# Kernel tuning notes

Hardware: AMD Instinct MI355X
Metric: run time of the kernel (lower is better)

## Reference

```python
import jax, jax.numpy as jnp
import numpy as np


def setup_inputs() -> dict:
    key = jax.random.key(0)
    k1, = jax.random.split(key, 1)
    B, L, D = 128, 1024, 768
    hidden_states = jax.random.normal(k1, (B, L, D), dtype=jnp.float32)
    attention_mask = jnp.zeros((B, 1, 1, L), dtype=jnp.float32)
    return {"hidden_states": hidden_states, "attention_mask": attention_mask, "K": 512}


def reference(hidden_states, attention_mask, K):
    B, L, D = hidden_states.shape
    # r tokens to merge, protected class token (ToMe: r = min(r, (t - protected)//2))
    r = max(0, L - K)
    r = min(r, (L - 1) // 2)

    # --- bipartite soft matching (indices computed under no_grad in torch) ---
    metric = hidden_states / jnp.linalg.norm(hidden_states, axis=-1, keepdims=True)
    a = metric[:, ::2, :]   # [B, t1, D] even tokens (src side)
    b = metric[:, 1::2, :]  # [B, t2, D] odd tokens (dst side)
    scores = jnp.einsum('bid,bjd->bij', a, b)  # [B, t1, t2]
    scores = scores.at[:, 0, :].set(-jnp.inf)  # protect class token (row 0 of src)
    node_max = jnp.max(scores, axis=-1)        # [B, t1]
    node_idx = jnp.argmax(scores, axis=-1)     # [B, t1] best dst per src
    order = jnp.argsort(-node_max, axis=-1)    # descending similarity
    src_idx = order[:, :r]                     # [B, r] tokens to merge away
    unm_idx = jnp.sort(order[:, r:], axis=-1)  # [B, t1-r] kept src tokens (sorted: class_token=True)
    dst_idx = jnp.take_along_axis(node_idx, src_idx, axis=-1)  # [B, r]

    # --- merge(x, mode='mean') with include_self=True ---
    src = hidden_states[:, ::2, :]   # [B, t1, D]
    dst = hidden_states[:, 1::2, :]  # [B, t2, D]
    t2 = dst.shape[1]
    unm = jnp.take_along_axis(src, unm_idx[..., None], axis=1)     # [B, t1-r, D]
    src_g = jnp.take_along_axis(src, src_idx[..., None], axis=1)   # [B, r, D]
    bidx = jnp.arange(B)[:, None]
    dst_sum = dst.at[bidx, dst_idx].add(src_g)                     # self + merged srcs
    counts = jnp.ones((B, t2), dtype=hidden_states.dtype).at[bidx, dst_idx].add(1.0)
    dst_mean = dst_sum / counts[..., None]

    preserved_tokens = jnp.concatenate([unm, dst_mean], axis=1)    # [B, t1-r+t2, D]
    final_attention_mask = jnp.zeros((B, 1, 1, preserved_tokens.shape[1]),
                                     dtype=hidden_states.dtype)
    return preserved_tokens, final_attention_mask
```

## Files before the change

### kernel.cpp

```cpp
#include <hip/hip_runtime.h>
#include <hip/hip_bf16.h>

#define B_ 128
#define L_ 1024
#define T_ 512
#define D_ 768
#define CH_ 96
#define DT_ 513
#define TAU_C 1e-3f
#define PBUF_ 1024

#define KS_B_CSTR 8208
#define KS_B_BYTES (4 * KS_B_CSTR)
#define KS_A_CSTR 1040
#define KS_A_BYTES (4 * KS_A_CSTR)
#define KS_BYTES (KS_B_BYTES + KS_A_BYTES)
#define SMEM_BYTES (4 * KS_BYTES)

typedef __attribute__((ext_vector_type(8))) short bf16x8;
typedef __attribute__((ext_vector_type(4))) float f32x4;

typedef const __attribute__((address_space(1))) unsigned int* gas1_t;
typedef __attribute__((address_space(3))) unsigned int* gas3_t;

__device__ __forceinline__ unsigned short f2bf_rne(float x){
    unsigned u = __float_as_uint(x);
    unsigned r = (u + 0x7FFFu + ((u >> 16) & 1u)) >> 16;
    return (unsigned short)r;
}

__global__ __launch_bounds__(256) void pack_k(const float* __restrict__ hs,
                                              unsigned short* __restrict__ Apk,
                                              unsigned short* __restrict__ Bpk,
                                              double* __restrict__ nsq,
                                              int* __restrict__ paircnt){
    __shared__ __align__(16) unsigned short LhS[CH_ * 16 * 8];
    if (blockIdx.x == 0 && threadIdx.x == 0) *paircnt = 0;
    int b = blockIdx.x >> 6, g = blockIdx.x & 63;
    int wv = threadIdx.x >> 6, lane = threadIdx.x & 63;

    #pragma unroll
    for (int rr = 0; rr < 4; ++rr){
        int jj = wv * 4 + rr;
        long seq = (long)b * L_ + g * 16 + jj;
        const float4* src = (const float4*)(hs + seq * D_);
        float4 f0 = src[lane], f1 = src[lane + 64], f2 = src[lane + 128];
        double s = 0.0;
        s += (double)f0.x*f0.x + (double)f0.y*f0.y + (double)f0.z*f0.z + (double)f0.w*f0.w;
        s += (double)f1.x*f1.x + (double)f1.y*f1.y + (double)f1.z*f1.z + (double)f1.w*f1.w;
        s += (double)f2.x*f2.x + (double)f2.y*f2.y + (double)f2.z*f2.z + (double)f2.w*f2.w;
        #pragma unroll
        for (int off = 32; off; off >>= 1) s += __shfl_xor(s, off);
        if (lane == 0 && (jj & 1)) nsq[seq] = s;
        float rn = (float)(1.0 / sqrt(s));
        float4 fv[3] = {f0, f1, f2};
        #pragma unroll
        for (int t = 0; t < 3; ++t){
            int e0 = t * 256 + lane * 4;
            int c = e0 >> 3, ei = e0 & 7;
            float vv[4] = {fv[t].x, fv[t].y, fv[t].z, fv[t].w};
            short4 hv;
            #pragma unroll
            for (int e = 0; e < 4; ++e)
                ((short*)&hv)[e] = (short)f2bf_rne(vv[e] * rn);
            int o = c * 128 + ((jj ^ (c & 7)) << 3) + ei;
            *(short4*)(LhS + o) = hv;
        }
    }
    __syncthreads();
    #pragma unroll
    for (int it = 0; it < 6; ++it){
        int linear = it * 256 + threadIdx.x;
        int c = linear >> 4, jj = linear & 15;
        int o = c * 128 + ((jj ^ (c & 7)) << 3);
        int tok = g * 8 + (jj >> 1);
        long go = ((long)(b * CH_ + c) * T_ + tok) * 8;
        if (jj & 1) *(bf16x8*)(Bpk + go) = *(const bf16x8*)(LhS + o);
        else        *(bf16x8*)(Apk + go) = *(const bf16x8*)(LhS + o);
    }
}

__global__ __launch_bounds__(512, 2) void coarse_k(const unsigned short* __restrict__ Apk,
                                                   const unsigned short* __restrict__ Bpk,
                                                   int* __restrict__ node_idx,
                                                   unsigned long long* __restrict__ rowkey,
                                                   int* __restrict__ paircnt,
                                                   int2* __restrict__ pairs){
    __shared__ __align__(16) char SMEM[SMEM_BYTES];

    int bid = blockIdx.x;
    int xcd = bid & 7, q = bid >> 3;
    int it = q & 7, bhi = q >> 3;
    int b = xcd + 8 * bhi;

    int tid = threadIdx.x;
    int w = tid >> 6, lane = tid & 63, l15 = lane & 15, l4 = lane >> 4;

    long pkbase = (long)b * CH_ * T_;
    int ca = w >> 1, tb4a = (w & 1) << 1;

    #define STAGE(s_, slot_) do {                                                          \
        char* dst_ = SMEM + (slot_) * KS_BYTES;                                            \
        _Pragma("unroll")                                                                  \
        for (int n_ = 0; n_ < 4; ++n_){                                                    \
            const unsigned short* sp_ = Bpk + (pkbase + (long)((s_)*4 + n_) * T_ + w * 64 + lane) * 8; \
            __builtin_amdgcn_global_load_lds((gas1_t)sp_, (gas3_t)(dst_ + n_ * KS_B_CSTR + w * 1024), 16, 0, 0); \
        }                                                                                  \
        _Pragma("unroll")                                                                  \
        for (int n_ = 0; n_ < 2; ++n_){                                                    \
            int tb_ = tb4a + n_;                                                           \
            const unsigned short* sp_ = Apk + (pkbase + (long)((s_)*4 + ca) * T_ + it * 64 + tb_ * 16) * 8 + lane * 2; \
            __builtin_amdgcn_global_load_lds((gas1_t)sp_, (gas3_t)(dst_ + KS_B_BYTES + ca * KS_A_CSTR + tb_ * 256), 4, 0, 0); \
        }                                                                                  \
    } while (0)

    STAGE(0, 0); STAGE(1, 1); STAGE(2, 2);

    f32x4 acc[4][4];
    #pragma unroll
    for (int i = 0; i < 4; ++i)
        #pragma unroll
        for (int j = 0; j < 4; ++j) acc[i][j] = (f32x4){0.f, 0.f, 0.f, 0.f};

    __syncthreads();

    #pragma unroll 4
    for (int s = 0; s < 24; ++s){
        if (s < 21) STAGE(s + 3, (s + 3) & 3);
        const char* slot = SMEM + (s & 3) * KS_BYTES;
        bf16x8 ah[4], bh[4];
        #pragma unroll
        for (int ib = 0; ib < 4; ++ib)
            ah[ib] = *(const bf16x8*)(slot + KS_B_BYTES + l4 * KS_A_CSTR + (ib * 16 + l15) * 16);
        #pragma unroll
        for (int jb = 0; jb < 4; ++jb)
            bh[jb] = *(const bf16x8*)(slot + l4 * KS_B_CSTR + (w * 64 + jb * 16 + l15) * 16);
        __builtin_amdgcn_s_setprio(1);
        #pragma unroll
        for (int jb = 0; jb < 4; ++jb)
            #pragma unroll
            for (int ib = 0; ib < 4; ++ib)
                acc[ib][jb] = __builtin_amdgcn_mfma_f32_16x16x32_bf16(ah[ib], bh[jb], acc[ib][jb], 0, 0, 0);
        __builtin_amdgcn_s_setprio(0);
        if (s <= 20)      asm volatile("s_waitcnt vmcnt(12)" ::: "memory");
        else if (s == 21) asm volatile("s_waitcnt vmcnt(6)"  ::: "memory");
        else              asm volatile("s_waitcnt vmcnt(0)"  ::: "memory");
        __builtin_amdgcn_s_barrier();
        asm volatile("" ::: "memory");
    }
    #undef STAGE

    float* pm1s = (float*)SMEM;
    int*   pjs  = (int*)(SMEM + 2048);
    float* m1f  = (float*)(SMEM + 4096);
    int*   cnd  = (int*)(SMEM + 4352);
    int2*  pbuf = (int2*)(SMEM + 4608);
    int*   pcnt_s  = (int*)(SMEM + 12800);
    int*   pbase_s = (int*)(SMEM + 12804);

    #pragma unroll
    for (int ib = 0; ib < 4; ++ib)
        #pragma unroll
        for (int rr = 0; rr < 4; ++rr){
            float m1 = -1e30f; int j1 = 0;
            #pragma unroll
            for (int jb = 0; jb < 4; ++jb){
                float v = acc[ib][jb][rr];
                int col = w * 64 + jb * 16 + l15;
                if (v > m1){ m1 = v; j1 = col; }
            }
            #pragma unroll
            for (int m = 1; m < 16; m <<= 1){
                float o1 = __shfl_xor(m1, m);
                int   oj = __shfl_xor(j1, m);
                if (o1 > m1 || (o1 == m1 && oj < j1)){ m1 = o1; j1 = oj; }
            }
            if (l15 == 0){
                int row = ib * 16 + l4 * 4 + rr;
                pm1s[row * 8 + w] = m1; pjs[row * 8 + w] = j1;
            }
        }
    __syncthreads();
    int grow0 = b * T_ + it * 64;
    if (tid < 64){
        float M1 = -1e30f; int J1 = 0;
        #pragma unroll
        for (int w2 = 0; w2 < 8; ++w2){
            float a1 = pm1s[tid * 8 + w2]; int aj = pjs[tid * 8 + w2];
            if (a1 > M1 || (a1 == M1 && aj < J1)){ M1 = a1; J1 = aj; }
        }
        node_idx[grow0 + tid] = J1;
        m1f[tid] = M1;
        cnd[tid] = 0;
        rowkey[grow0 + tid] = 0ULL;
        if (tid == 0) *pcnt_s = 0;
    }
    __syncthreads();
    #pragma unroll
    for (int ib = 0; ib < 4; ++ib)
        #pragma unroll
        for (int rr = 0; rr < 4; ++rr){
            int row = ib * 16 + l4 * 4 + rr;
            float thr_ = m1f[row] - TAU_C;
            int hits = 0;
            #pragma unroll
            for (int jb = 0; jb < 4; ++jb) hits += (acc[ib][jb][rr] > thr_) ? 1 : 0;
            #pragma unroll
            for (int m = 1; m < 16; m <<= 1) hits += __shfl_xor(hits, m);
            if (l15 == 0 && hits) atomicAdd(&cnd[row], hits);
        }
    __syncthreads();
    #pragma unroll
    for (int ib = 0; ib < 4; ++ib)
        #pragma unroll
        for (int rr = 0; rr < 4; ++rr){
            int row = ib * 16 + l4 * 4 + rr;
            if (cnd[row] < 2) continue;
            if (it == 0 && row == 0) continue;
            float thr_ = m1f[row] - TAU_C;
            #pragma unroll
            for (int jb = 0; jb < 4; ++jb)
                if (acc[ib][jb][rr] > thr_){
                    int idx = atomicAdd(pcnt_s, 1);
                    int2 pr = make_int2(grow0 + row, w * 64 + jb * 16 + l15);
                    if (idx < PBUF_) pbuf[idx] = pr;
                    else { int p = atomicAdd(paircnt, 1); pairs[p] = pr; }
                }
        }
    __syncthreads();
    if (tid == 0) *pbase_s = atomicAdd(paircnt, min(*pcnt_s, PBUF_));
    __syncthreads();
    int n = min(*pcnt_s, PBUF_);
    for (int k2 = tid; k2 < n; k2 += 512) pairs[*pbase_s + k2] = pbuf[k2];
}

__global__ __launch_bounds__(256) void refine_k(const float* __restrict__ hs,
                                                const double* __restrict__ nsq,
                                                const int* __restrict__ paircnt,
                                                const int2* __restrict__ pairs,
                                                unsigned long long* __restrict__ rowkey){
    int n = *paircnt;
    int w = threadIdx.x >> 6, lane = threadIdx.x & 63;
    for (int p = blockIdx.x * 4 + w; p < n; p += gridDim.x * 4){
        int2 pr = pairs[p];
        int grow = pr.x, j = pr.y;
        int b = grow >> 9, i = grow & 511;
        const float* ar = hs + ((long)b * L_ + 2 * i) * D_;
        const float* br = hs + ((long)b * L_ + 2 * j + 1) * D_;
        double s = 0.0;
        #pragma unroll
        for (int dd = 0; dd < 12; ++dd){
            int d = dd * 64 + lane;
            s += (double)ar[d] * (double)br[d];
        }
        #pragma unroll
        for (int off = 32; off; off >>= 1) s += __shfl_xor(s, off);
        if (lane == 0){
            double sc = s / sqrt(nsq[(long)b * L_ + 2 * j + 1]);
            unsigned long long bits = (unsigned long long)__double_as_longlong(sc);
            unsigned long long key = (bits >> 63) ? ~bits : (bits | 0x8000000000000000ULL);
            key = (key & ~0xFFFFULL) | (unsigned long long)(511 - j);
            atomicMax(&rowkey[grow], key);
        }
    }
}

__global__ __launch_bounds__(512) void csr_k(const int* __restrict__ node_idx,
                                             const unsigned long long* __restrict__ rowkey,
                                             int* __restrict__ goff,
                                             int* __restrict__ glist){
    __shared__ int sidx[512];
    __shared__ int off[513];
    __shared__ int tmp[512];
    __shared__ int cnt[512];
    int b = blockIdx.x, t = threadIdx.x;
    unsigned long long rk = rowkey[b * T_ + t];
    sidx[t] = rk ? (511 - (int)(rk & 0xFFFFULL)) : node_idx[b * T_ + t];
    cnt[t] = 0;
    __syncthreads();
    if (t >= 1) atomicAdd(&cnt[sidx[t]], 1);
    __syncthreads();
    tmp[t] = cnt[t];
    __syncthreads();
    for (int s = 1; s < 512; s <<= 1){
        int v = (t >= s) ? tmp[t - s] : 0;
        __syncthreads();
        tmp[t] += v;
        __syncthreads();
    }
    if (t == 0) off[0] = 0;
    off[t + 1] = tmp[t];
    __syncthreads();
    if (t >= 1){
        int j = sidx[t], r = 0;
        for (int i2 = 1; i2 < t; ++i2) r += (sidx[i2] == j);
        glist[b * T_ + off[j] + r] = t;
    }
    goff[b * 513 + t] = off[t];
    if (t == 0) goff[b * 513 + 512] = off[512];
}

__global__ __launch_bounds__(192) void merge_k(const float* __restrict__ hs,
                                               const int* __restrict__ goff,
                                               const int* __restrict__ glist,
                                               float* __restrict__ out){
    int bid = blockIdx.x;
    int b = bid / DT_, jj = bid - b * DT_;
    long obase4 = ((long)b * DT_ + jj) * (D_ / 4);
    float4* out4 = (float4*)out;
    if (threadIdx.x == 0) out[(long)B_ * DT_ * D_ + b * DT_ + jj] = 0.0f;
    int d = threadIdx.x;
    if (jj == 0){
        const float4* src = (const float4*)(hs + (long)b * L_ * D_);
        out4[obase4 + d] = src[d];
        return;
    }
    int j = jj - 1;
    int o0 = goff[b * 513 + j], o1 = goff[b * 513 + j + 1];
    const float4* dst = (const float4*)(hs + ((long)b * L_ + 2 * j + 1) * D_);
    float4 a = dst[d];
    for (int s = o0; s < o1; ++s){
        int i = glist[b * T_ + s];
        const float4* srow = (const float4*)(hs + ((long)b * L_ + 2 * i) * D_);
        float4 v = srow[d];
        a.x += v.x; a.y += v.y; a.z += v.z; a.w += v.w;
    }
    float rc = 1.0f / (float)(o1 - o0 + 1);
    a.x *= rc; a.y *= rc; a.z *= rc; a.w *= rc;
    out4[obase4 + d] = a;
}

extern "C" void kernel_launch(void* const* d_in, const int* in_sizes, int n_in,
                              void* d_out, int out_size, void* d_ws, size_t ws_size,
                              hipStream_t stream){
    const float* hs = (const float*)d_in[0];
    float* out = (float*)d_out;
    char* ws = (char*)d_ws;

    const long PSZ = (long)B_ * CH_ * T_ * 8;
    unsigned short* Apk = (unsigned short*)ws;
    unsigned short* Bpk = Apk + PSZ;
    double* nsq      = (double*)(ws + 201326592);
    int*    node_idx = (int*)   (ws + 202375168);
    unsigned long long* rowkey = (unsigned long long*)(ws + 202637312);
    int*    paircnt  = (int*)   (ws + 203161600);
    int*    goff     = (int*)   (ws + 203161856);
    int*    glist    = (int*)   (ws + 203425024);
    int2*   pairs    = (int2*)  (ws + 203687168);

    pack_k  <<<B_ * 64, 256, 0, stream>>>(hs, Apk, Bpk, nsq, paircnt);
    coarse_k<<<B_ * 8, 512, 0, stream>>>(Apk, Bpk, node_idx, rowkey, paircnt, pairs);
    refine_k<<<512, 256, 0, stream>>>(hs, nsq, paircnt, pairs, rowkey);
    csr_k   <<<B_, 512, 0, stream>>>(node_idx, rowkey, goff, glist);
    merge_k <<<B_ * DT_, 192, 0, stream>>>(hs, goff, glist, out);
}
```

Measured before the change: 365.7 us.

## Enlarge coarse GEMM row tile to 128 with 2x4 wave grid and triple buffering

Each coarse_k block now handles 128 src rows instead of 64. The 8 waves form a 2x4 grid, each computing a 64x128 accumulator tile, so each B-chunk staged into LDS is reused across twice as many rows and the grid shrinks to 512 blocks. The A tile is loaded with 16-byte global_load_lds, and the pipeline drops from four stages to three to fit LDS, with the vmcnt waits adjusted to match. Doubling the accumulators raises register pressure and may hurt occupancy, and the shallower pipeline hides less load latency.

```diff
diff --git a/kernel.cpp b/kernel.cpp
--- a/kernel.cpp
+++ b/kernel.cpp
@@ -12,10 +12,10 @@
 
 #define KS_B_CSTR 8208
 #define KS_B_BYTES (4 * KS_B_CSTR)
-#define KS_A_CSTR 1040
+#define KS_A_CSTR 2064
 #define KS_A_BYTES (4 * KS_A_CSTR)
 #define KS_BYTES (KS_B_BYTES + KS_A_BYTES)
-#define SMEM_BYTES (4 * KS_BYTES)
+#define SMEM_BYTES (3 * KS_BYTES)
 
 typedef __attribute__((ext_vector_type(8))) short bf16x8;
 typedef __attribute__((ext_vector_type(4))) float f32x4;
@@ -90,14 +90,14 @@
 
     int bid = blockIdx.x;
     int xcd = bid & 7, q = bid >> 3;
-    int it = q & 7, bhi = q >> 3;
+    int it = q & 3, bhi = q >> 2;
     int b = xcd + 8 * bhi;
 
     int tid = threadIdx.x;
     int w = tid >> 6, lane = tid & 63, l15 = lane & 15, l4 = lane >> 4;
+    int wr = w >> 2, wc = w & 3;
 
     long pkbase = (long)b * CH_ * T_;
-    int ca = w >> 1, tb4a = (w & 1) << 1;
 
     #define STAGE(s_, slot_) do {                                                          \
         char* dst_ = SMEM + (slot_) * KS_BYTES;                                            \
@@ -106,45 +106,42 @@
             const unsigned short* sp_ = Bpk + (pkbase + (long)((s_)*4 + n_) * T_ + w * 64 + lane) * 8; \
             __builtin_amdgcn_global_load_lds((gas1_t)sp_, (gas3_t)(dst_ + n_ * KS_B_CSTR + w * 1024), 16, 0, 0); \
         }                                                                                  \
-        _Pragma("unroll")                                                                  \
-        for (int n_ = 0; n_ < 2; ++n_){                                                    \
-            int tb_ = tb4a + n_;                                                           \
-            const unsigned short* sp_ = Apk + (pkbase + (long)((s_)*4 + ca) * T_ + it * 64 + tb_ * 16) * 8 + lane * 2; \
-            __builtin_amdgcn_global_load_lds((gas1_t)sp_, (gas3_t)(dst_ + KS_B_BYTES + ca * KS_A_CSTR + tb_ * 256), 4, 0, 0); \
+        {                                                                                  \
+            const unsigned short* sp_ = Apk + (pkbase + (long)((s_)*4 + (w >> 1)) * T_ + it * 128 + (w & 1) * 64 + lane) * 8; \
+            __builtin_amdgcn_global_load_lds((gas1_t)sp_, (gas3_t)(dst_ + KS_B_BYTES + (w >> 1) * KS_A_CSTR + (w & 1) * 1024), 16, 0, 0); \
         }                                                                                  \
     } while (0)
 
-    STAGE(0, 0); STAGE(1, 1); STAGE(2, 2);
-
-    f32x4 acc[4][4];
+    STAGE(0, 0); STAGE(1, 1);
+
+    f32x4 acc[4][8];
     #pragma unroll
     for (int i = 0; i < 4; ++i)
         #pragma unroll
-        for (int j = 0; j < 4; ++j) acc[i][j] = (f32x4){0.f, 0.f, 0.f, 0.f};
-
-    __syncthreads();
-
-    #pragma unroll 4
+        for (int j = 0; j < 8; ++j) acc[i][j] = (f32x4){0.f, 0.f, 0.f, 0.f};
+
+    __syncthreads();
+
+    #pragma unroll 3
     for (int s = 0; s < 24; ++s){
-        if (s < 21) STAGE(s + 3, (s + 3) & 3);
-        const char* slot = SMEM + (s & 3) * KS_BYTES;
-        bf16x8 ah[4], bh[4];
+        if (s < 22) STAGE(s + 2, (s + 2) % 3);
+        const char* slot = SMEM + (s % 3) * KS_BYTES;
+        bf16x8 ah[4], bh[8];
         #pragma unroll
         for (int ib = 0; ib < 4; ++ib)
-            ah[ib] = *(const bf16x8*)(slot + KS_B_BYTES + l4 * KS_A_CSTR + (ib * 16 + l15) * 16);
-        #pragma unroll
-        for (int jb = 0; jb < 4; ++jb)
-            bh[jb] = *(const bf16x8*)(slot + l4 * KS_B_CSTR + (w * 64 + jb * 16 + l15) * 16);
+            ah[ib] = *(const bf16x8*)(slot + KS_B_BYTES + l4 * KS_A_CSTR + (wr * 64 + ib * 16 + l15) * 16);
+        #pragma unroll
+        for (int jb = 0; jb < 8; ++jb)
+            bh[jb] = *(const bf16x8*)(slot + l4 * KS_B_CSTR + (wc * 128 + jb * 16 + l15) * 16);
         __builtin_amdgcn_s_setprio(1);
         #pragma unroll
-        for (int jb = 0; jb < 4; ++jb)
+        for (int jb = 0; jb < 8; ++jb)
             #pragma unroll
             for (int ib = 0; ib < 4; ++ib)
                 acc[ib][jb] = __builtin_amdgcn_mfma_f32_16x16x32_bf16(ah[ib], bh[jb], acc[ib][jb], 0, 0, 0);
         __builtin_amdgcn_s_setprio(0);
-        if (s <= 20)      asm volatile("s_waitcnt vmcnt(12)" ::: "memory");
-        else if (s == 21) asm volatile("s_waitcnt vmcnt(6)"  ::: "memory");
-        else              asm volatile("s_waitcnt vmcnt(0)"  ::: "memory");
+        if (s < 22)      asm volatile("s_waitcnt vmcnt(5)" ::: "memory");
+        else             asm volatile("s_waitcnt vmcnt(0)" ::: "memory");
         __builtin_amdgcn_s_barrier();
         asm volatile("" ::: "memory");
     }
@@ -153,10 +150,10 @@
     float* pm1s = (float*)SMEM;
     int*   pjs  = (int*)(SMEM + 2048);
     float* m1f  = (float*)(SMEM + 4096);
-    int*   cnd  = (int*)(SMEM + 4352);
-    int2*  pbuf = (int2*)(SMEM + 4608);
-    int*   pcnt_s  = (int*)(SMEM + 12800);
-    int*   pbase_s = (int*)(SMEM + 12804);
+    int*   cnd  = (int*)(SMEM + 4608);
+    int2*  pbuf = (int2*)(SMEM + 5120);
+    int*   pcnt_s  = (int*)(SMEM + 13312);
+    int*   pbase_s = (int*)(SMEM + 13316);
 
     #pragma unroll
     for (int ib = 0; ib < 4; ++ib)
@@ -164,9 +161,9 @@
         for (int rr = 0; rr < 4; ++rr){
             float m1 = -1e30f; int j1 = 0;
             #pragma unroll
-            for (int jb = 0; jb < 4; ++jb){
+            for (int jb = 0; jb < 8; ++jb){
                 float v = acc[ib][jb][rr];
-                int col = w * 64 + jb * 16 + l15;
+                int col = wc * 128 + jb * 16 + l15;
                 if (v > m1){ m1 = v; j1 = col; }
             }
             #pragma unroll
@@ -176,17 +173,17 @@
                 if (o1 > m1 || (o1 == m1 && oj < j1)){ m1 = o1; j1 = oj; }
             }
             if (l15 == 0){
-                int row = ib * 16 + l4 * 4 + rr;
-                pm1s[row * 8 + w] = m1; pjs[row * 8 + w] = j1;
+                int row = wr * 64 + ib * 16 + l4 * 4 + rr;
+                pm1s[row * 4 + wc] = m1; pjs[row * 4 + wc] = j1;
             }
         }
     __syncthreads();
-    int grow0 = b * T_ + it * 64;
-    if (tid < 64){
+    int grow0 = b * T_ + it * 128;
+    if (tid < 128){
         float M1 = -1e30f; int J1 = 0;
         #pragma unroll
-        for (int w2 = 0; w2 < 8; ++w2){
-            float a1 = pm1s[tid * 8 + w2]; int aj = pjs[tid * 8 + w2];
+        for (int c2 = 0; c2 < 4; ++c2){
+            float a1 = pm1s[tid * 4 + c2]; int aj = pjs[tid * 4 + c2];
             if (a1 > M1 || (a1 == M1 && aj < J1)){ M1 = a1; J1 = aj; }
         }
         node_idx[grow0 + tid] = J1;
@@ -200,11 +197,11 @@
     for (int ib = 0; ib < 4; ++ib)
         #pragma unroll
         for (int rr = 0; rr < 4; ++rr){
-            int row = ib * 16 + l4 * 4 + rr;
+            int row = wr * 64 + ib * 16 + l4 * 4 + rr;
             float thr_ = m1f[row] - TAU_C;
             int hits = 0;
             #pragma unroll
-            for (int jb = 0; jb < 4; ++jb) hits += (acc[ib][jb][rr] > thr_) ? 1 : 0;
+            for (int jb = 0; jb < 8; ++jb) hits += (acc[ib][jb][rr] > thr_) ? 1 : 0;
             #pragma unroll
             for (int m = 1; m < 16; m <<= 1) hits += __shfl_xor(hits, m);
             if (l15 == 0 && hits) atomicAdd(&cnd[row], hits);
@@ -214,15 +211,15 @@
     for (int ib = 0; ib < 4; ++ib)
         #pragma unroll
         for (int rr = 0; rr < 4; ++rr){
-            int row = ib * 16 + l4 * 4 + rr;
+            int row = wr * 64 + ib * 16 + l4 * 4 + rr;
             if (cnd[row] < 2) continue;
             if (it == 0 && row == 0) continue;
             float thr_ = m1f[row] - TAU_C;
             #pragma unroll
-            for (int jb = 0; jb < 4; ++jb)
+            for (int jb = 0; jb < 8; ++jb)
                 if (acc[ib][jb][rr] > thr_){
                     int idx = atomicAdd(pcnt_s, 1);
-                    int2 pr = make_int2(grow0 + row, w * 64 + jb * 16 + l15);
+                    int2 pr = make_int2(grow0 + row, wc * 128 + jb * 16 + l15);
                     if (idx < PBUF_) pbuf[idx] = pr;
                     else { int p = atomicAdd(paircnt, 1); pairs[p] = pr; }
                 }
@@ -349,7 +346,7 @@
     int2*   pairs    = (int2*)  (ws + 203687168);
 
     pack_k  <<<B_ * 64, 256, 0, stream>>>(hs, Apk, Bpk, nsq, paircnt);
-    coarse_k<<<B_ * 8, 512, 0, stream>>>(Apk, Bpk, node_idx, rowkey, paircnt, pairs);
+    coarse_k<<<512, 512, 0, stream>>>(Apk, Bpk, node_idx, rowkey, paircnt, pairs);
     refine_k<<<512, 256, 0, stream>>>(hs, nsq, paircnt, pairs, rowkey);
     csr_k   <<<B_, 512, 0, stream>>>(node_idx, rowkey, goff, glist);
     merge_k <<<B_ * DT_, 192, 0, stream>>>(hs, goff, glist, out);
```

Measured after the change: 328.5 us (median of 2 runs). 10.2% less time.
